# Optimization experiments

Hardware: AMD Instinct MI355X
Metric: run time of the kernel (lower is better)

The kernel has to match this reference:

```python
import jax, jax.numpy as jnp
import numpy as np

NUM_HEADS = 8
EPS = 1e-9


def setup_inputs() -> dict:
    key = jax.random.key(0)
    ks = jax.random.split(key, 5)
    B, S, D = 2, 2048, 512
    x = jax.random.normal(ks[0], (B, S, D), dtype=jnp.float32)
    Wq = jax.random.normal(ks[1], (D, D), dtype=jnp.float32) * (1.0 / np.sqrt(D))
    Wk = jax.random.normal(ks[2], (D, D), dtype=jnp.float32) * (1.0 / np.sqrt(D))
    Wv = jax.random.normal(ks[3], (D, D), dtype=jnp.float32) * (1.0 / np.sqrt(D))
    Wo = jax.random.normal(ks[4], (D, D), dtype=jnp.float32) * (1.0 / np.sqrt(D))
    gamma = jnp.ones((D,), dtype=jnp.float32)
    beta = jnp.zeros((D,), dtype=jnp.float32)
    return {"x": x, "Wq": Wq, "Wk": Wk, "Wv": Wv, "Wo": Wo, "gamma": gamma, "beta": beta}


def _layernorm(x, gamma, beta):
    mean = jnp.mean(x, axis=-1, keepdims=True)
    var = jnp.mean(jnp.square(x - mean), axis=-1, keepdims=True)
    return gamma * ((x - mean) * jax.lax.rsqrt(var + EPS)) + beta


def reference(x, Wq, Wk, Wv, Wo, gamma, beta):
    B, S, D = x.shape
    H = NUM_HEADS
    dh = D // H
    # Note: in the original, K_V=(inputs, inputs) is captured BEFORE LayerNorm,
    # so only Q is layer-normalized; K and V use the raw inputs.
    q_in = _layernorm(x, gamma, beta)
    Q = jnp.einsum('bsd,de->bse', q_in, Wq).reshape(B, S, H, dh)
    K = jnp.einsum('bsd,de->bse', x, Wk).reshape(B, S, H, dh)
    V = jnp.einsum('bsd,de->bse', x, Wv).reshape(B, S, H, dh)
    # scaled dot-product attention (bias = 0, dropout disabled since dropout=1)
    scores = jnp.einsum('bqhd,bkhd->bhqk', Q, K) / jnp.sqrt(jnp.float32(dh))
    attn = jax.nn.softmax(scores, axis=-1)
    ctx = jnp.einsum('bhqk,bkhd->bqhd', attn, V).reshape(B, S, D)
    out = jnp.einsum('bsd,de->bse', ctx, Wo) + x  # output proj + residual
    return out
```

## Files before the change

kernel.cpp:

```cpp
#include <hip/hip_runtime.h>

typedef __bf16 bf16x8 __attribute__((ext_vector_type(8)));
typedef float f32x4 __attribute__((ext_vector_type(4)));

#define SCALE_LOG2E 0.18033688011112042f

__device__ __forceinline__ float bf2f(unsigned int u) { return __uint_as_float(u << 16); }
__device__ __forceinline__ unsigned short f2bfu(float f) {
    union { __bf16 h; unsigned short u; } v;
    v.h = (__bf16)f;
    return v.u;
}
__device__ __forceinline__ unsigned int pk2bf(float a, float b) {
    union { __bf16 h[2]; unsigned int u; } v;
    v.h[0] = (__bf16)a; v.h[1] = (__bf16)b;
    return v.u;
}

__device__ int probe_bf16(const void* xp) {
    const unsigned short* u = (const unsigned short*)xp;
    int cnt = 0;
    for (int i = 0; i < 128; i++) {
        unsigned e = (u[i] >> 7) & 0xFFu;
        cnt += (e == 0u || (e >= 0x6Cu && e <= 0x8Au)) ? 1 : 0;
    }
    return cnt >= 120;
}

__global__ __launch_bounds__(64)
void probe_k(const void* __restrict__ x, const void* __restrict__ Wq, int* __restrict__ flags) {
    if (threadIdx.x == 0) {
        flags[0] = probe_bf16(x);
        flags[1] = probe_bf16(Wq);
    }
}

__device__ __forceinline__ void load8f(const void* p, int isb, size_t idx, float* o) {
    if (isb) {
        uint4 v = *(const uint4*)((const unsigned short*)p + idx);
        o[0] = bf2f(v.x & 0xffffu); o[1] = bf2f(v.x >> 16);
        o[2] = bf2f(v.y & 0xffffu); o[3] = bf2f(v.y >> 16);
        o[4] = bf2f(v.z & 0xffffu); o[5] = bf2f(v.z >> 16);
        o[6] = bf2f(v.w & 0xffffu); o[7] = bf2f(v.w >> 16);
    } else {
        const float* f = (const float*)p + idx;
        float4 a = *(const float4*)f;
        float4 b = *(const float4*)(f + 4);
        o[0] = a.x; o[1] = a.y; o[2] = a.z; o[3] = a.w;
        o[4] = b.x; o[5] = b.y; o[6] = b.z; o[7] = b.w;
    }
}
__device__ __forceinline__ void load2f(const void* p, int isb, size_t idx, float& a, float& b) {
    if (isb) {
        unsigned int v = *(const unsigned int*)((const unsigned short*)p + idx);
        a = bf2f(v & 0xffffu); b = bf2f(v >> 16);
    } else {
        float2 f = *(const float2*)((const float*)p + idx);
        a = f.x; b = f.y;
    }
}
__device__ __forceinline__ float load1f(const void* p, int isb, size_t idx) {
    return isb ? bf2f((unsigned int)((const unsigned short*)p)[idx]) : ((const float*)p)[idx];
}

__global__ __launch_bounds__(256)
void setup_k(const void* __restrict__ x, const void* __restrict__ Wq, const void* __restrict__ Wk,
             const void* __restrict__ Wv, const void* __restrict__ Wo,
             const void* __restrict__ gamma, const void* __restrict__ beta,
             float* __restrict__ rowstats, float* __restrict__ gf, float* __restrict__ bfv,
             unsigned short* __restrict__ WT, const int* __restrict__ flags) {
    const int t = threadIdx.x;
    const int bid = blockIdx.x;
    if (bid < 1024) {
        const int isb = flags[1];
        __shared__ float tile[32][33];
        const int which = bid >> 8, tl = bid & 255;
        const int bx = (tl & 15) * 32, by = (tl >> 4) * 32;
        const void* W = (which == 0) ? Wq : (which == 1) ? Wk : (which == 2) ? Wv : Wo;
        unsigned short* dst = WT + (size_t)which * 512 * 512;
        const int xx = t & 31, y0 = t >> 5;
#pragma unroll
        for (int i = 0; i < 4; i++) {
            int y = y0 + i * 8;
            tile[y][xx] = load1f(W, isb, (size_t)(by + y) * 512 + bx + xx);
        }
        __syncthreads();
#pragma unroll
        for (int i = 0; i < 4; i++) {
            int y = y0 + i * 8;
            dst[(size_t)(bx + y) * 512 + by + xx] = f2bfu(tile[xx][y]);
        }
        return;
    }
    const int isb = flags[0];
    if (bid >= 5120) {
        const void* src = (bid == 5120) ? gamma : beta;
        float* dst = (bid == 5120) ? gf : bfv;
        float a, b;
        load2f(src, isb, (size_t)t * 2, a, b);
        dst[t * 2] = a; dst[t * 2 + 1] = b;
        return;
    }
    const int row = bid - 1024;
    float a, b;
    load2f(x, isb, (size_t)row * 512 + t * 2, a, b);
    float s = a + b, sq = a * a + b * b;
#pragma unroll
    for (int msk = 1; msk < 64; msk <<= 1) {
        s += __shfl_xor(s, msk);
        sq += __shfl_xor(sq, msk);
    }
    __shared__ float red[8];
    if ((t & 63) == 0) { red[t >> 6] = s; red[4 + (t >> 6)] = sq; }
    __syncthreads();
    if (t == 0) {
        float S = red[0] + red[1] + red[2] + red[3];
        float SQ = red[4] + red[5] + red[6] + red[7];
        float mean = S * (1.0f / 512.0f);
        float var = SQ * (1.0f / 512.0f) - mean * mean;
        rowstats[2 * row] = mean;
        rowstats[2 * row + 1] = rsqrtf(fmaxf(var, 0.0f) + 1e-9f);
    }
}

__global__ __launch_bounds__(256)
void proj_all_k(const void* __restrict__ x, const unsigned short* __restrict__ WT,
                const float* __restrict__ rowstats, const float* __restrict__ gf,
                const float* __restrict__ bfv, unsigned short* __restrict__ Qb,
                unsigned short* __restrict__ Kb, unsigned short* __restrict__ VtF,
                const int* __restrict__ flags) {
    __shared__ unsigned short As[128 * 40];
    __shared__ unsigned short Bs[128 * 40];
    __shared__ float Gs[512], Bts[512];
    const int t = threadIdx.x;
    const int isb = flags[0];
    const int w = t >> 6, lane = t & 63;
    const int quad = lane >> 4, ln = lane & 15;

    if (blockIdx.z == 0) {
        const int role = blockIdx.x & 1;
        const int n0 = (blockIdx.x >> 1) * 128;
        const int m0 = blockIdx.y * 128;
        const unsigned short* BT = WT + (size_t)role * 512 * 512;
        unsigned short* out = role ? Kb : Qb;
        const int wm = w & 1, wn = w >> 1;
        Gs[t] = gf[t]; Gs[t + 256] = gf[t + 256];
        Bts[t] = bfv[t]; Bts[t + 256] = bfv[t + 256];

        f32x4 acc[4][4];
        const f32x4 zero = {0.f, 0.f, 0.f, 0.f};
#pragma unroll
        for (int i = 0; i < 4; i++)
#pragma unroll
            for (int j = 0; j < 4; j++) acc[i][j] = zero;

        for (int kt = 0; kt < 512; kt += 32) {
            __syncthreads();
#pragma unroll
            for (int i = 0; i < 2; i++) {
                int o = t + i * 256;
                int r = o >> 2, c8 = o & 3;
                size_t gidx = (size_t)(m0 + r) * 512 + kt + c8 * 8;
                if (isb && role == 1) {
                    *(uint4*)(&As[r * 40 + c8 * 8]) = *(const uint4*)((const unsigned short*)x + gidx);
                } else {
                    float f[8];
                    load8f(x, isb, gidx, f);
                    if (role == 0) {
                        float mean = rowstats[2 * (m0 + r)];
                        float inv = rowstats[2 * (m0 + r) + 1];
#pragma unroll
                        for (int j = 0; j < 8; j++) {
                            int k = kt + c8 * 8 + j;
                            f[j] = (f[j] - mean) * inv * Gs[k] + Bts[k];
                        }
                    }
                    unsigned int pk[4];
#pragma unroll
                    for (int j = 0; j < 4; j++) pk[j] = pk2bf(f[2 * j], f[2 * j + 1]);
                    *(uint4*)(&As[r * 40 + c8 * 8]) = make_uint4(pk[0], pk[1], pk[2], pk[3]);
                }
                *(uint4*)(&Bs[r * 40 + c8 * 8]) = *(const uint4*)(BT + (size_t)(n0 + r) * 512 + kt + c8 * 8);
            }
            __syncthreads();
            bf16x8 af[4], bfr[4];
#pragma unroll
            for (int i = 0; i < 4; i++) {
                af[i] = *(const bf16x8*)(&As[(wm * 64 + i * 16 + ln) * 40 + quad * 8]);
                bfr[i] = *(const bf16x8*)(&Bs[(wn * 64 + i * 16 + ln) * 40 + quad * 8]);
            }
#pragma unroll
            for (int i = 0; i < 4; i++)
#pragma unroll
                for (int j = 0; j < 4; j++)
                    acc[i][j] = __builtin_amdgcn_mfma_f32_16x16x32_bf16(af[i], bfr[j], acc[i][j], 0, 0, 0);
        }
#pragma unroll
        for (int i = 0; i < 4; i++)
#pragma unroll
            for (int j = 0; j < 4; j++)
#pragma unroll
                for (int r = 0; r < 4; r++) {
                    int grow = m0 + wm * 64 + i * 16 + quad * 4 + r;
                    int gcol = n0 + wn * 64 + j * 16 + ln;
                    float v = acc[i][j][r];
                    if (role == 0) v *= SCALE_LOG2E;
                    out[(size_t)grow * 512 + gcol] = f2bfu(v);
                }
    } else {
        const int m0 = blockIdx.x * 64;
        const int n0 = blockIdx.y * 128;
        const unsigned short* AW = WT + (size_t)2 * 512 * 512;

        f32x4 acc[8];
        const f32x4 zero = {0.f, 0.f, 0.f, 0.f};
#pragma unroll
        for (int j = 0; j < 8; j++) acc[j] = zero;

        for (int kt = 0; kt < 512; kt += 32) {
            __syncthreads();
            {
                int r = t >> 2, c8 = t & 3;
                *(uint4*)(&As[r * 40 + c8 * 8]) = *(const uint4*)(AW + (size_t)(m0 + r) * 512 + kt + c8 * 8);
            }
#pragma unroll
            for (int i = 0; i < 2; i++) {
                int o = t + i * 256;
                int r = o >> 2, c8 = o & 3;
                size_t gidx = (size_t)(n0 + r) * 512 + kt + c8 * 8;
                if (isb) {
                    *(uint4*)(&Bs[r * 40 + c8 * 8]) = *(const uint4*)((const unsigned short*)x + gidx);
                } else {
                    float f[8];
                    load8f(x, isb, gidx, f);
                    unsigned int pk[4];
#pragma unroll
                    for (int j = 0; j < 4; j++) pk[j] = pk2bf(f[2 * j], f[2 * j + 1]);
                    *(uint4*)(&Bs[r * 40 + c8 * 8]) = make_uint4(pk[0], pk[1], pk[2], pk[3]);
                }
            }
            __syncthreads();
            bf16x8 af = *(const bf16x8*)(&As[(w * 16 + ln) * 40 + quad * 8]);
#pragma unroll
            for (int j = 0; j < 8; j++) {
                bf16x8 bfr = *(const bf16x8*)(&Bs[(j * 16 + ln) * 40 + quad * 8]);
                acc[j] = __builtin_amdgcn_mfma_f32_16x16x32_bf16(af, bfr, acc[j], 0, 0, 0);
            }
        }
#pragma unroll
        for (int j = 0; j < 8; j++)
#pragma unroll
            for (int r = 0; r < 4; r++) {
                int grow = m0 + w * 16 + quad * 4 + r;
                int gcol = n0 + j * 16 + ln;
                VtF[(size_t)grow * 4096 + gcol] = f2bfu(acc[j][r]);
            }
    }
}

__global__ __launch_bounds__(1024, 1)
void attn_m_k(const unsigned short* __restrict__ Qb, const unsigned short* __restrict__ Kb,
              const unsigned short* __restrict__ VtF, unsigned short* __restrict__ ctx) {
    const int S = 2048, PT = 72, NT = 32;
    const int t = threadIdx.x;
    const int qb = blockIdx.x, h = blockIdx.y, b = blockIdx.z;
    const int w = t >> 6, lane = t & 63;
    const int quad = lane >> 4, ln = lane & 15;
    const int kq = w & 3, qh = w >> 2;

    __shared__ unsigned short sh[27648];
    unsigned short* const KsA = sh;
    unsigned short* const KsB = sh + 4608;
    unsigned short* const Vt0 = sh + 9216;
    unsigned short* const Vt1 = sh + 13824;
    unsigned short* const Vt2 = sh + 18432;
    unsigned short* const Vt3 = sh + 23040;
    unsigned short* const Qs  = sh + 18432;

    const size_t baseQ  = (size_t)(b * S + qb * 128) * 512 + h * 64;
    const size_t baseK  = (size_t)(b * S) * 512 + h * 64;
    const size_t baseVt = (size_t)(h * 64) * 4096 + (size_t)b * S;

    const int c8 = t & 7;
    const int r64 = (t & 511) >> 3;
    const int stoff = r64 * PT + c8 * 8;

    const int kfo0 = (kq * 16 + ln) * PT + quad * 8;
    const int vto  = ln * PT + kq * 16 + quad * 4;

    const unsigned short* const gK = Kb + baseK + (size_t)r64 * 512 + c8 * 8;
    const unsigned short* const gV = VtF + baseVt + (size_t)r64 * 4096 + c8 * 8;

    uint4 sa, sb;
    if (t < 512) { sa = *(const uint4*)(gK); sb = *(const uint4*)(gK + 32768); }
    else         { sa = *(const uint4*)(gV); sb = *(const uint4*)(gV + 64); }

    {
        const int rQ = t >> 3;
        *(uint4*)(&Qs[rQ * PT + c8 * 8]) = *(const uint4*)(Qb + baseQ + (size_t)rQ * 512 + c8 * 8);
    }
    __syncthreads();
    bf16x8 qf[2][2];
#pragma unroll
    for (int s2 = 0; s2 < 2; s2++)
#pragma unroll
        for (int i = 0; i < 2; i++)
            qf[s2][i] = *(const bf16x8*)(&Qs[(qh * 32 + s2 * 16 + ln) * PT + quad * 8 + 32 * i]);

    f32x4 acc[2][4];
    const f32x4 zero = {0.f, 0.f, 0.f, 0.f};
#pragma unroll
    for (int s2 = 0; s2 < 2; s2++)
#pragma unroll
        for (int j = 0; j < 4; j++) acc[s2][j] = zero;
    float lsum0 = 0.f, lsum1 = 0.f;

#define STAGE(KS, VT, R)                                                    \
    {                                                                       \
        if (t < 512) *(uint4*)(&KS[stoff]) = R;                             \
        else         *(uint4*)(&VT[stoff]) = R;                             \
    }
#define PRELOAD(R, kt)                                                      \
    if ((kt) < NT) {                                                        \
        if (t < 512) R = *(const uint4*)(gK + (size_t)(kt) * 32768);        \
        else         R = *(const uint4*)(gV + (size_t)(kt) * 64);           \
    }
#define QK_EXP(KS, U00, U01, U10, U11)                                      \
    {                                                                       \
        bf16x8 kf0 = *(const bf16x8*)(&KS[kfo0]);                           \
        bf16x8 kf1 = *(const bf16x8*)(&KS[kfo0 + 32]);                      \
        f32x4 sc0 = zero, sc1 = zero;                                       \
        sc0 = __builtin_amdgcn_mfma_f32_16x16x32_bf16(kf0, qf[0][0], sc0, 0, 0, 0); \
        sc0 = __builtin_amdgcn_mfma_f32_16x16x32_bf16(kf1, qf[0][1], sc0, 0, 0, 0); \
        sc1 = __builtin_amdgcn_mfma_f32_16x16x32_bf16(kf0, qf[1][0], sc1, 0, 0, 0); \
        sc1 = __builtin_amdgcn_mfma_f32_16x16x32_bf16(kf1, qf[1][1], sc1, 0, 0, 0); \
        float a0 = __builtin_amdgcn_exp2f(fminf(sc0[0], 30.f));             \
        float a1 = __builtin_amdgcn_exp2f(fminf(sc0[1], 30.f));             \
        float a2 = __builtin_amdgcn_exp2f(fminf(sc0[2], 30.f));             \
        float a3 = __builtin_amdgcn_exp2f(fminf(sc0[3], 30.f));             \
        lsum0 += (a0 + a1) + (a2 + a3);                                     \
        U00 = pk2bf(a0, a1); U01 = pk2bf(a2, a3);                           \
        float b0 = __builtin_amdgcn_exp2f(fminf(sc1[0], 30.f));             \
        float b1 = __builtin_amdgcn_exp2f(fminf(sc1[1], 30.f));             \
        float b2 = __builtin_amdgcn_exp2f(fminf(sc1[2], 30.f));             \
        float b3 = __builtin_amdgcn_exp2f(fminf(sc1[3], 30.f));             \
        lsum1 += (b0 + b1) + (b2 + b3);                                     \
        U10 = pk2bf(b0, b1); U11 = pk2bf(b2, b3);                           \
    }
#define PV4(VTE, VTO)                                                       \
    {                                                                       \
        bf16x8 ap0 = __builtin_bit_cast(bf16x8, make_uint4(uA00, uA01, uB00, uB01)); \
        bf16x8 ap1 = __builtin_bit_cast(bf16x8, make_uint4(uA10, uA11, uB10, uB11)); \
        _Pragma("unroll")                                                   \
        for (int nt = 0; nt < 4; nt++) {                                    \
            uint2 ve = *(const uint2*)(&VTE[vto + nt * 16 * PT]);           \
            uint2 vo = *(const uint2*)(&VTO[vto + nt * 16 * PT]);           \
            bf16x8 vb = __builtin_bit_cast(bf16x8, make_uint4(ve.x, ve.y, vo.x, vo.y)); \
            acc[0][nt] = __builtin_amdgcn_mfma_f32_16x16x32_bf16(ap0, vb, acc[0][nt], 0, 0, 0); \
            acc[1][nt] = __builtin_amdgcn_mfma_f32_16x16x32_bf16(ap1, vb, acc[1][nt], 0, 0, 0); \
        }                                                                   \
    }

    for (int m = 0; m < 8; m++) {
        const int T = m * 4;
        unsigned int uA00, uA01, uA10, uA11, uB00, uB01, uB10, uB11;
        STAGE(KsA, Vt0, sa);
        __syncthreads();
        PRELOAD(sa, T + 2);
        QK_EXP(KsA, uA00, uA01, uA10, uA11);
        STAGE(KsB, Vt1, sb);
        __syncthreads();
        PRELOAD(sb, T + 3);
        QK_EXP(KsB, uB00, uB01, uB10, uB11);
        PV4(Vt0, Vt1);
        STAGE(KsA, Vt2, sa);
        __syncthreads();
        PRELOAD(sa, T + 4);
        QK_EXP(KsA, uA00, uA01, uA10, uA11);
        STAGE(KsB, Vt3, sb);
        __syncthreads();
        PRELOAD(sb, T + 5);
        QK_EXP(KsB, uB00, uB01, uB10, uB11);
        PV4(Vt2, Vt3);
    }
#undef STAGE
#undef PRELOAD
#undef QK_EXP
#undef PV4

    lsum0 += __shfl_xor(lsum0, 16);
    lsum0 += __shfl_xor(lsum0, 32);
    lsum1 += __shfl_xor(lsum1, 16);
    lsum1 += __shfl_xor(lsum1, 32);

    __syncthreads();
    float* scr  = (float*)sh;
    float* lred = scr + 13056;
    if (quad == 0) {
        lred[kq * 128 + qh * 32 + ln] = lsum0;
        lred[kq * 128 + qh * 32 + 16 + ln] = lsum1;
    }
#pragma unroll
    for (int rr = 0; rr < 2; rr++) {
        __syncthreads();
        if ((qh >> 1) == rr && kq != 0) {
            const int pb = (kq - 1) * 4352 + ((qh & 1) * 32 + quad * 4) * 68 + ln;
#pragma unroll
            for (int s2 = 0; s2 < 2; s2++)
#pragma unroll
                for (int nt = 0; nt < 4; nt++)
#pragma unroll
                    for (int r = 0; r < 4; r++)
                        scr[pb + (s2 * 16 + r) * 68 + nt * 16] = acc[s2][nt][r];
        }
        __syncthreads();
        if ((qh >> 1) == rr && kq == 0) {
#pragma unroll
            for (int s2 = 0; s2 < 2; s2++) {
                const size_t baseO = (size_t)(b * S + qb * 128 + qh * 32 + s2 * 16 + quad * 4) * 512 + h * 64 + ln;
#pragma unroll
                for (int r = 0; r < 4; r++) {
                    int qrow = qh * 32 + s2 * 16 + quad * 4 + r;
                    float lt = lred[qrow] + lred[128 + qrow] + lred[256 + qrow] + lred[384 + qrow];
                    float inv = 1.0f / lt;
                    int rb = ((qh & 1) * 32 + s2 * 16 + quad * 4 + r) * 68 + ln;
#pragma unroll
                    for (int nt = 0; nt < 4; nt++) {
                        float v = acc[s2][nt][r] + scr[rb + nt * 16] + scr[4352 + rb + nt * 16] + scr[8704 + rb + nt * 16];
                        ctx[baseO + (size_t)r * 512 + nt * 16] = f2bfu(v * inv);
                    }
                }
            }
        }
    }
}

__global__ __launch_bounds__(256)
void outproj_k(const unsigned short* __restrict__ ctx, const unsigned short* __restrict__ BT,
               const void* __restrict__ x, void* __restrict__ outp, const int* __restrict__ flags) {
    __shared__ unsigned short As[128 * 40];
    __shared__ unsigned short Bs[64 * 40];
    const int t = threadIdx.x;
    const int isb = flags[0];
    const int m0 = blockIdx.y * 128, n0 = blockIdx.x * 64;
    const int w = t >> 6, lane = t & 63;
    const int wm = w & 1, wn = w >> 1;
    const int quad = lane >> 4, ln = lane & 15;

    f32x4 acc[4][2];
    const f32x4 zero = {0.f, 0.f, 0.f, 0.f};
#pragma unroll
    for (int i = 0; i < 4; i++)
#pragma unroll
        for (int j = 0; j < 2; j++) acc[i][j] = zero;

    for (int kt = 0; kt < 512; kt += 32) {
        __syncthreads();
#pragma unroll
        for (int i = 0; i < 2; i++) {
            int o = t + i * 256;
            int r = o >> 2, c8 = o & 3;
            *(uint4*)(&As[r * 40 + c8 * 8]) = *(const uint4*)(ctx + (size_t)(m0 + r) * 512 + kt + c8 * 8);
        }
        {
            int r = t >> 2, c8 = t & 3;
            *(uint4*)(&Bs[r * 40 + c8 * 8]) = *(const uint4*)(BT + (size_t)(n0 + r) * 512 + kt + c8 * 8);
        }
        __syncthreads();
        bf16x8 af[4], bfr[2];
#pragma unroll
        for (int i = 0; i < 4; i++)
            af[i] = *(const bf16x8*)(&As[(wm * 64 + i * 16 + ln) * 40 + quad * 8]);
#pragma unroll
        for (int j = 0; j < 2; j++)
            bfr[j] = *(const bf16x8*)(&Bs[(wn * 32 + j * 16 + ln) * 40 + quad * 8]);
#pragma unroll
        for (int i = 0; i < 4; i++)
#pragma unroll
            for (int j = 0; j < 2; j++)
                acc[i][j] = __builtin_amdgcn_mfma_f32_16x16x32_bf16(af[i], bfr[j], acc[i][j], 0, 0, 0);
    }
#pragma unroll
    for (int i = 0; i < 4; i++)
#pragma unroll
        for (int j = 0; j < 2; j++)
#pragma unroll
            for (int r = 0; r < 4; r++) {
                int grow = m0 + wm * 64 + i * 16 + quad * 4 + r;
                int gcol = n0 + wn * 32 + j * 16 + ln;
                size_t idx = (size_t)grow * 512 + gcol;
                float v = acc[i][j][r] + load1f(x, isb, idx);
                if (isb) ((unsigned short*)outp)[idx] = f2bfu(v);
                else     ((float*)outp)[idx] = v;
            }
}

__global__ __launch_bounds__(256)
void fill_k(unsigned short* out, int n) {
    int i = blockIdx.x * 256 + threadIdx.x;
    if (i < n) out[i] = 0x4442;
}

extern "C" void kernel_launch(void* const* d_in, const int* in_sizes, int n_in,
                              void* d_out, int out_size, void* d_ws, size_t ws_size,
                              hipStream_t stream) {
    const void* x     = d_in[0];
    const void* Wq    = d_in[1];
    const void* Wk    = d_in[2];
    const void* Wv    = d_in[3];
    const void* Wo    = d_in[4];
    const void* gamma = d_in[5];
    const void* beta  = d_in[6];

    const size_t NW = 512 * 512;
    const size_t NX = 4096 * 512;
    char* w = (char*)d_ws;

    const size_t FULL_STATS_OFF = 2097152 + 3 * NX * 2;
    const size_t NEED_FULL = FULL_STATS_OFF + 32768 + 4096 + 16;

    if (ws_size < NEED_FULL) {
        fill_k<<<(out_size + 255) / 256, 256, 0, stream>>>((unsigned short*)d_out, out_size);
        return;
    }

    unsigned short* WT  = (unsigned short*)w;
    unsigned short* Qb  = (unsigned short*)(w + 2097152);
    unsigned short* Kb  = Qb + NX;
    unsigned short* VtF = Kb + NX;
    unsigned short* ctx = Qb;
    float* rowstats = (float*)(w + FULL_STATS_OFF);
    float* gf = rowstats + 8192;
    float* bfv = gf + 512;
    int* flags = (int*)(bfv + 512);

    probe_k<<<1, 64, 0, stream>>>(x, Wq, flags);
    setup_k<<<5122, 256, 0, stream>>>(x, Wq, Wk, Wv, Wo, gamma, beta, rowstats, gf, bfv, WT, flags);
    proj_all_k<<<dim3(8, 32, 2), 256, 0, stream>>>(x, WT, rowstats, gf, bfv, Qb, Kb, VtF, flags);
    attn_m_k<<<dim3(16, 8, 2), 1024, 0, stream>>>(Qb, Kb, VtF, ctx);
    outproj_k<<<dim3(8, 32), 256, 0, stream>>>(ctx, WT + 3 * NW, x, d_out, flags);
}
```

Before: 161.0 us.

## Fold dtype probe into setup kernel and shrink projection tiles for more blocks

Removes the separate single-thread probe launch: each setup block now runs the bf16 probe on the inputs itself, and one block writes the flags for later kernels. The Q/K and V projection tiles are halved (128x64 and 64x64), with the grid flattened to 1024 blocks. The output projection tile is also reduced to 64x64, doubling its grid. This aims to cut launch overhead and fill more CUs, at the cost of redundant probe reads in every setup block and less data reuse per tile.

```diff
diff --git a/kernel.cpp b/kernel.cpp
--- a/kernel.cpp
+++ b/kernel.cpp
@@ -25,14 +25,6 @@
         cnt += (e == 0u || (e >= 0x6Cu && e <= 0x8Au)) ? 1 : 0;
     }
     return cnt >= 120;
-}
-
-__global__ __launch_bounds__(64)
-void probe_k(const void* __restrict__ x, const void* __restrict__ Wq, int* __restrict__ flags) {
-    if (threadIdx.x == 0) {
-        flags[0] = probe_bf16(x);
-        flags[1] = probe_bf16(Wq);
-    }
 }
 
 __device__ __forceinline__ void load8f(const void* p, int isb, size_t idx, float* o) {
@@ -68,11 +60,11 @@
              const void* __restrict__ Wv, const void* __restrict__ Wo,
              const void* __restrict__ gamma, const void* __restrict__ beta,
              float* __restrict__ rowstats, float* __restrict__ gf, float* __restrict__ bfv,
-             unsigned short* __restrict__ WT, const int* __restrict__ flags) {
+             unsigned short* __restrict__ WT, int* __restrict__ flags) {
     const int t = threadIdx.x;
     const int bid = blockIdx.x;
     if (bid < 1024) {
-        const int isb = flags[1];
+        const int isb = probe_bf16(Wq);
         __shared__ float tile[32][33];
         const int which = bid >> 8, tl = bid & 255;
         const int bx = (tl & 15) * 32, by = (tl >> 4) * 32;
@@ -92,13 +84,17 @@
         }
         return;
     }
-    const int isb = flags[0];
+    const int isb = probe_bf16(x);
     if (bid >= 5120) {
         const void* src = (bid == 5120) ? gamma : beta;
         float* dst = (bid == 5120) ? gf : bfv;
         float a, b;
         load2f(src, isb, (size_t)t * 2, a, b);
         dst[t * 2] = a; dst[t * 2 + 1] = b;
+        if (bid == 5121 && t == 0) {
+            flags[0] = isb;
+            flags[1] = probe_bf16(Wq);
+        }
         return;
     }
     const int row = bid - 1024;
@@ -130,27 +126,30 @@
                 unsigned short* __restrict__ Kb, unsigned short* __restrict__ VtF,
                 const int* __restrict__ flags) {
     __shared__ unsigned short As[128 * 40];
-    __shared__ unsigned short Bs[128 * 40];
+    __shared__ unsigned short Bs[64 * 40];
     __shared__ float Gs[512], Bts[512];
     const int t = threadIdx.x;
     const int isb = flags[0];
     const int w = t >> 6, lane = t & 63;
     const int quad = lane >> 4, ln = lane & 15;
-
-    if (blockIdx.z == 0) {
-        const int role = blockIdx.x & 1;
-        const int n0 = (blockIdx.x >> 1) * 128;
-        const int m0 = blockIdx.y * 128;
+    const int bid = blockIdx.x;
+    const f32x4 zero = {0.f, 0.f, 0.f, 0.f};
+
+    if (bid < 512) {
+        const int xi = bid & 15;
+        const int role = xi & 1;
+        const int n0 = (xi >> 1) * 64;
+        const int m0 = (bid >> 4) * 128;
         const unsigned short* BT = WT + (size_t)role * 512 * 512;
         unsigned short* out = role ? Kb : Qb;
-        const int wm = w & 1, wn = w >> 1;
-        Gs[t] = gf[t]; Gs[t + 256] = gf[t + 256];
-        Bts[t] = bfv[t]; Bts[t + 256] = bfv[t + 256];
-
-        f32x4 acc[4][4];
-        const f32x4 zero = {0.f, 0.f, 0.f, 0.f};
-#pragma unroll
-        for (int i = 0; i < 4; i++)
+        if (role == 0) {
+            Gs[t] = gf[t]; Gs[t + 256] = gf[t + 256];
+            Bts[t] = bfv[t]; Bts[t + 256] = bfv[t + 256];
+        }
+
+        f32x4 acc[2][4];
+#pragma unroll
+        for (int i = 0; i < 2; i++)
 #pragma unroll
             for (int j = 0; j < 4; j++) acc[i][j] = zero;
 
@@ -180,42 +179,46 @@
                     for (int j = 0; j < 4; j++) pk[j] = pk2bf(f[2 * j], f[2 * j + 1]);
                     *(uint4*)(&As[r * 40 + c8 * 8]) = make_uint4(pk[0], pk[1], pk[2], pk[3]);
                 }
+            }
+            {
+                int r = t >> 2, c8 = t & 3;
                 *(uint4*)(&Bs[r * 40 + c8 * 8]) = *(const uint4*)(BT + (size_t)(n0 + r) * 512 + kt + c8 * 8);
             }
             __syncthreads();
-            bf16x8 af[4], bfr[4];
-#pragma unroll
-            for (int i = 0; i < 4; i++) {
-                af[i] = *(const bf16x8*)(&As[(wm * 64 + i * 16 + ln) * 40 + quad * 8]);
-                bfr[i] = *(const bf16x8*)(&Bs[(wn * 64 + i * 16 + ln) * 40 + quad * 8]);
-            }
-#pragma unroll
-            for (int i = 0; i < 4; i++)
+            bf16x8 af[2], bfr[4];
+#pragma unroll
+            for (int i = 0; i < 2; i++)
+                af[i] = *(const bf16x8*)(&As[(w * 32 + i * 16 + ln) * 40 + quad * 8]);
+#pragma unroll
+            for (int j = 0; j < 4; j++)
+                bfr[j] = *(const bf16x8*)(&Bs[(j * 16 + ln) * 40 + quad * 8]);
+#pragma unroll
+            for (int i = 0; i < 2; i++)
 #pragma unroll
                 for (int j = 0; j < 4; j++)
                     acc[i][j] = __builtin_amdgcn_mfma_f32_16x16x32_bf16(af[i], bfr[j], acc[i][j], 0, 0, 0);
         }
 #pragma unroll
-        for (int i = 0; i < 4; i++)
+        for (int i = 0; i < 2; i++)
 #pragma unroll
             for (int j = 0; j < 4; j++)
 #pragma unroll
                 for (int r = 0; r < 4; r++) {
-                    int grow = m0 + wm * 64 + i * 16 + quad * 4 + r;
-                    int gcol = n0 + wn * 64 + j * 16 + ln;
+                    int grow = m0 + w * 32 + i * 16 + quad * 4 + r;
+                    int gcol = n0 + j * 16 + ln;
                     float v = acc[i][j][r];
                     if (role == 0) v *= SCALE_LOG2E;
                     out[(size_t)grow * 512 + gcol] = f2bfu(v);
                 }
     } else {
-        const int m0 = blockIdx.x * 64;
-        const int n0 = blockIdx.y * 128;
+        const int idx = bid - 512;
+        const int m0 = (idx & 7) * 64;
+        const int n0 = (idx >> 3) * 64;
         const unsigned short* AW = WT + (size_t)2 * 512 * 512;
 
-        f32x4 acc[8];
-        const f32x4 zero = {0.f, 0.f, 0.f, 0.f};
-#pragma unroll
-        for (int j = 0; j < 8; j++) acc[j] = zero;
+        f32x4 acc[4];
+#pragma unroll
+        for (int j = 0; j < 4; j++) acc[j] = zero;
 
         for (int kt = 0; kt < 512; kt += 32) {
             __syncthreads();
@@ -223,10 +226,8 @@
                 int r = t >> 2, c8 = t & 3;
                 *(uint4*)(&As[r * 40 + c8 * 8]) = *(const uint4*)(AW + (size_t)(m0 + r) * 512 + kt + c8 * 8);
             }
-#pragma unroll
-            for (int i = 0; i < 2; i++) {
-                int o = t + i * 256;
-                int r = o >> 2, c8 = o & 3;
+            {
+                int r = t >> 2, c8 = t & 3;
                 size_t gidx = (size_t)(n0 + r) * 512 + kt + c8 * 8;
                 if (isb) {
                     *(uint4*)(&Bs[r * 40 + c8 * 8]) = *(const uint4*)((const unsigned short*)x + gidx);
@@ -242,13 +243,13 @@
             __syncthreads();
             bf16x8 af = *(const bf16x8*)(&As[(w * 16 + ln) * 40 + quad * 8]);
 #pragma unroll
-            for (int j = 0; j < 8; j++) {
+            for (int j = 0; j < 4; j++) {
                 bf16x8 bfr = *(const bf16x8*)(&Bs[(j * 16 + ln) * 40 + quad * 8]);
                 acc[j] = __builtin_amdgcn_mfma_f32_16x16x32_bf16(af, bfr, acc[j], 0, 0, 0);
             }
         }
 #pragma unroll
-        for (int j = 0; j < 8; j++)
+        for (int j = 0; j < 4; j++)
 #pragma unroll
             for (int r = 0; r < 4; r++) {
                 int grow = m0 + w * 16 + quad * 4 + r;
@@ -438,61 +439,45 @@
 __global__ __launch_bounds__(256)
 void outproj_k(const unsigned short* __restrict__ ctx, const unsigned short* __restrict__ BT,
                const void* __restrict__ x, void* __restrict__ outp, const int* __restrict__ flags) {
-    __shared__ unsigned short As[128 * 40];
+    __shared__ unsigned short As[64 * 40];
     __shared__ unsigned short Bs[64 * 40];
     const int t = threadIdx.x;
     const int isb = flags[0];
-    const int m0 = blockIdx.y * 128, n0 = blockIdx.x * 64;
+    const int m0 = blockIdx.y * 64, n0 = blockIdx.x * 64;
     const int w = t >> 6, lane = t & 63;
-    const int wm = w & 1, wn = w >> 1;
     const int quad = lane >> 4, ln = lane & 15;
 
-    f32x4 acc[4][2];
+    f32x4 acc[4];
     const f32x4 zero = {0.f, 0.f, 0.f, 0.f};
 #pragma unroll
-    for (int i = 0; i < 4; i++)
-#pragma unroll
-        for (int j = 0; j < 2; j++) acc[i][j] = zero;
+    for (int j = 0; j < 4; j++) acc[j] = zero;
 
     for (int kt = 0; kt < 512; kt += 32) {
         __syncthreads();
-#pragma unroll
-        for (int i = 0; i < 2; i++) {
-            int o = t + i * 256;
-            int r = o >> 2, c8 = o & 3;
-            *(uint4*)(&As[r * 40 + c8 * 8]) = *(const uint4*)(ctx + (size_t)(m0 + r) * 512 + kt + c8 * 8);
-        }
         {
             int r = t >> 2, c8 = t & 3;
+            *(uint4*)(&As[r * 40 + c8 * 8]) = *(const uint4*)(ctx + (size_t)(m0 + r) * 512 + kt + c8 * 8);
             *(uint4*)(&Bs[r * 40 + c8 * 8]) = *(const uint4*)(BT + (size_t)(n0 + r) * 512 + kt + c8 * 8);
         }
         __syncthreads();
-        bf16x8 af[4], bfr[2];
-#pragma unroll
-        for (int i = 0; i < 4; i++)
-            af[i] = *(const bf16x8*)(&As[(wm * 64 + i * 16 + ln) * 40 + quad * 8]);
-#pragma unroll
-        for (int j = 0; j < 2; j++)
-            bfr[j] = *(const bf16x8*)(&Bs[(wn * 32 + j * 16 + ln) * 40 + quad * 8]);
-#pragma unroll
-        for (int i = 0; i < 4; i++)
-#pragma unroll
-            for (int j = 0; j < 2; j++)
-                acc[i][j] = __builtin_amdgcn_mfma_f32_16x16x32_bf16(af[i], bfr[j], acc[i][j], 0, 0, 0);
-    }
-#pragma unroll
-    for (int i = 0; i < 4; i++)
-#pragma unroll
-        for (int j = 0; j < 2; j++)
-#pragma unroll
-            for (int r = 0; r < 4; r++) {
-                int grow = m0 + wm * 64 + i * 16 + quad * 4 + r;
-                int gcol = n0 + wn * 32 + j * 16 + ln;
-                size_t idx = (size_t)grow * 512 + gcol;
-                float v = acc[i][j][r] + load1f(x, isb, idx);
-                if (isb) ((unsigned short*)outp)[idx] = f2bfu(v);
-                else     ((float*)outp)[idx] = v;
-            }
+        bf16x8 af = *(const bf16x8*)(&As[(w * 16 + ln) * 40 + quad * 8]);
+#pragma unroll
+        for (int j = 0; j < 4; j++) {
+            bf16x8 bfr = *(const bf16x8*)(&Bs[(j * 16 + ln) * 40 + quad * 8]);
+            acc[j] = __builtin_amdgcn_mfma_f32_16x16x32_bf16(af, bfr, acc[j], 0, 0, 0);
+        }
+    }
+#pragma unroll
+    for (int j = 0; j < 4; j++)
+#pragma unroll
+        for (int r = 0; r < 4; r++) {
+            int grow = m0 + w * 16 + quad * 4 + r;
+            int gcol = n0 + j * 16 + ln;
+            size_t idx = (size_t)grow * 512 + gcol;
+            float v = acc[j][r] + load1f(x, isb, idx);
+            if (isb) ((unsigned short*)outp)[idx] = f2bfu(v);
+            else     ((float*)outp)[idx] = v;
+        }
 }
 
 __global__ __launch_bounds__(256)
@@ -534,9 +519,8 @@
     float* bfv = gf + 512;
     int* flags = (int*)(bfv + 512);
 
-    probe_k<<<1, 64, 0, stream>>>(x, Wq, flags);
     setup_k<<<5122, 256, 0, stream>>>(x, Wq, Wk, Wv, Wo, gamma, beta, rowstats, gf, bfv, WT, flags);
-    proj_all_k<<<dim3(8, 32, 2), 256, 0, stream>>>(x, WT, rowstats, gf, bfv, Qb, Kb, VtF, flags);
+    proj_all_k<<<1024, 256, 0, stream>>>(x, WT, rowstats, gf, bfv, Qb, Kb, VtF, flags);
     attn_m_k<<<dim3(16, 8, 2), 1024, 0, stream>>>(Qb, Kb, VtF, ctx);
-    outproj_k<<<dim3(8, 32), 256, 0, stream>>>(ctx, WT + 3 * NW, x, d_out, flags);
-}
+    outproj_k<<<dim3(8, 64), 256, 0, stream>>>(ctx, WT + 3 * NW, x, d_out, flags);
+}
```

Result: slower. 174.6 us (+8.4%).
